# Kernel tuning notes

Hardware: AMD Instinct MI355X
Metric: run time of the kernel (lower is better)

## Reference

```python
import jax, jax.numpy as jnp
import numpy as np

IN_FEAT = 3 * 32 * 32  # channels*height*width
HID = 1024
CLASSES = 10
EPS = 1e-5


def binarize(w):
    # Deterministic BinaryConnect: sign(w) in {-1, +1} (sign(0) -> +1)
    return jnp.where(w >= 0, 1.0, -1.0).astype(w.dtype)


def batchnorm(h, gamma, beta):
    # training-mode BatchNorm1d: biased batch stats over batch axis
    mean = jnp.mean(h, axis=0)
    var = jnp.var(h, axis=0)
    return gamma * (h - mean) * jax.lax.rsqrt(var + EPS) + beta


def setup_inputs() -> dict:
    key = jax.random.key(0)
    ks = jax.random.split(key, 6)
    x = jax.random.normal(ks[0], (8192, 3, 32, 32), dtype=jnp.float32)
    # latent real-valued weights, torch Linear layout [out, in], kaiming-ish scale
    W1 = jax.random.normal(ks[1], (HID, IN_FEAT), dtype=jnp.float32) * (1.0 / np.sqrt(IN_FEAT))
    W2 = jax.random.normal(ks[2], (HID, HID), dtype=jnp.float32) * (1.0 / np.sqrt(HID))
    W3 = jax.random.normal(ks[3], (HID, HID), dtype=jnp.float32) * (1.0 / np.sqrt(HID))
    W4 = jax.random.normal(ks[4], (CLASSES, HID), dtype=jnp.float32) * (1.0 / np.sqrt(HID))
    g1 = jnp.ones((HID,), jnp.float32); b1 = jnp.zeros((HID,), jnp.float32)
    g2 = jnp.ones((HID,), jnp.float32); b2 = jnp.zeros((HID,), jnp.float32)
    g3 = jnp.ones((HID,), jnp.float32); b3 = jnp.zeros((HID,), jnp.float32)
    return {"x": x, "W1": W1, "W2": W2, "W3": W3, "W4": W4,
            "g1": g1, "b1": b1, "g2": g2, "b2": b2, "g3": g3, "b3": b3}


def reference(x, W1, W2, W3, W4, g1, b1, g2, b2, g3, b3):
    h = x.reshape(-1, IN_FEAT)                       # [B, 3072]
    h = jax.nn.relu(h @ binarize(W1).T)              # [B, 1024]
    h = batchnorm(h, g1, b1)
    h = jax.nn.relu(h @ binarize(W2).T)
    h = batchnorm(h, g2, b2)
    h = jax.nn.relu(h @ binarize(W3).T)
    h = batchnorm(h, g3, b3)
    return h @ binarize(W4).T                        # [B, classes]
```

## Files before the change

### kernel.cpp

```cpp
#include <hip/hip_runtime.h>
#include <stdint.h>

typedef unsigned short u16;
typedef __attribute__((ext_vector_type(8))) unsigned short ushort8;
typedef __attribute__((ext_vector_type(4))) unsigned short ushort4v;
typedef __attribute__((ext_vector_type(8))) __bf16 bf16x8;
typedef __attribute__((ext_vector_type(4))) float f32x4;
typedef __attribute__((ext_vector_type(16))) float f32x16;

__device__ __forceinline__ u16 f2bf(float f) {
    union { float f; unsigned int u; } v; v.f = f;
    unsigned int r = v.u + 0x7FFFu + ((v.u >> 16) & 1u);
    return (u16)(r >> 16);
}
__device__ __forceinline__ float bf2f(u16 b) {
    union { unsigned int u; float f; } v; v.u = ((unsigned int)b) << 16;
    return v.f;
}

typedef __attribute__((address_space(1))) const uint32_t* gptr_t;
typedef __attribute__((address_space(3))) uint32_t* lptr_t;
__device__ __forceinline__ void async_copy16(const void* g, void* l) {
    __builtin_amdgcn_global_load_lds((gptr_t)g, (lptr_t)l, 16, 0, 0);
}


__global__ __launch_bounds__(256) void pre_kernel(
    const float* __restrict__ x, const float* __restrict__ W1,
    const float* __restrict__ W4,
    u16* __restrict__ Xb, u16* __restrict__ W1b, u16* __restrict__ W4T)
{
    const int b = blockIdx.x;
    if (b < 12288) {
        int i = b * 256 + threadIdx.x;
        const float4* p = (const float4*)(x + (size_t)i * 8);
        float4 x0 = p[0], x1 = p[1];
        ushort8 o;
        o[0] = f2bf(x0.x); o[1] = f2bf(x0.y); o[2] = f2bf(x0.z); o[3] = f2bf(x0.w);
        o[4] = f2bf(x1.x); o[5] = f2bf(x1.y); o[6] = f2bf(x1.z); o[7] = f2bf(x1.w);
        *(ushort8*)(Xb + (size_t)i * 8) = o;
    } else if (b < 13824) {
        int i = (b - 12288) * 256 + threadIdx.x;
        const float4* p = (const float4*)(W1 + (size_t)i * 8);
        float4 x0 = p[0], x1 = p[1];
        ushort8 o;
        o[0] = x0.x >= 0.f ? 0x3F80 : 0xBF80;
        o[1] = x0.y >= 0.f ? 0x3F80 : 0xBF80;
        o[2] = x0.z >= 0.f ? 0x3F80 : 0xBF80;
        o[3] = x0.w >= 0.f ? 0x3F80 : 0xBF80;
        o[4] = x1.x >= 0.f ? 0x3F80 : 0xBF80;
        o[5] = x1.y >= 0.f ? 0x3F80 : 0xBF80;
        o[6] = x1.z >= 0.f ? 0x3F80 : 0xBF80;
        o[7] = x1.w >= 0.f ? 0x3F80 : 0xBF80;
        *(ushort8*)(W1b + (size_t)i * 8) = o;
    } else {
        int idx = (b - 13824) * 256 + threadIdx.x;
        int k = idx >> 4, c = idx & 15;
        u16 v = 0;
        if (c < 10) v = (W4[(size_t)c * 1024 + k] >= 0.f) ? 0x3F80 : 0xBF80;
        W4T[idx] = v;
    }
}

__global__ __launch_bounds__(256) void rescale_w(
    const float* __restrict__ W, const float* __restrict__ ss,
    u16* __restrict__ Wp, float* __restrict__ bias)
{
    const int lane = threadIdx.x & 63;
    const int wid  = threadIdx.x >> 6;
    const int r    = blockIdx.x * 4 + wid;
    float bsum = 0.f;
    #pragma unroll
    for (int k0 = 0; k0 < 1024; k0 += 256) {
        int k = k0 + lane * 4;
        float4 w  = *(const float4*)(W + (size_t)r * 1024 + k);
        float4 sc = *(const float4*)(ss + k);
        float4 sh = *(const float4*)(ss + 1024 + k);
        ushort4v o;
        o[0] = f2bf(w.x >= 0.f ? sc.x : -sc.x);
        o[1] = f2bf(w.y >= 0.f ? sc.y : -sc.y);
        o[2] = f2bf(w.z >= 0.f ? sc.z : -sc.z);
        o[3] = f2bf(w.w >= 0.f ? sc.w : -sc.w);
        bsum += (w.x >= 0.f ? sh.x : -sh.x) + (w.y >= 0.f ? sh.y : -sh.y)
              + (w.z >= 0.f ? sh.z : -sh.z) + (w.w >= 0.f ? sh.w : -sh.w);
        *(ushort4v*)(Wp + (size_t)r * 1024 + k) = o;
    }
    #pragma unroll
    for (int off = 32; off; off >>= 1) bsum += __shfl_xor(bsum, off, 64);
    if (lane == 0) bias[r] = bsum;
}

__device__ __forceinline__ void xcd_map(int& mm, int& jj) {
    const int d = blockIdx.x + blockIdx.y * gridDim.x;
    mm = (d & 7) + (d >> 6) * 8;
    jj = (d >> 3) & 7;
}


__global__ __launch_bounds__(256) void gemm_fused(
    const u16* __restrict__ A, const u16* __restrict__ B,
    u16* __restrict__ H, const float* __restrict__ bias,
    float* __restrict__ partS, float* __restrict__ partS2,
    int M, int N, int K)
{
    __shared__ __align__(16) u16 As[2][128 * 64];
    __shared__ __align__(16) u16 Bs[2][128 * 64];

    const int tid  = threadIdx.x;
    const int wid  = tid >> 6;
    const int lane = tid & 63;
    const int cl   = lane & 31;
    const int hi   = lane >> 5;
    const int x7r  = cl & 7;
    const int wr   = wid >> 1;
    const int wc   = wid & 1;

    int mm, jj;
    xcd_map(mm, jj);
    const int row0 = mm * 128;
    const int col0 = jj * 128;

    const int s_r = tid >> 3;
    const int s_c = (((tid & 7) ^ (s_r & 7)) << 3);
    const u16* gA = A + (size_t)(row0 + s_r) * K + s_c;
    const u16* gB = B + (size_t)(col0 + s_r) * K + s_c;

    const int a_base0 = (wr * 64 +  0 + cl) * 64;
    const int a_base1 = (wr * 64 + 32 + cl) * 64;
    const int b_base0 = (wc * 64 +  0 + cl) * 64;
    const int b_base1 = (wc * 64 + 32 + cl) * 64;

    f32x16 acc[2][2];
    #pragma unroll
    for (int i = 0; i < 2; ++i)
        #pragma unroll
        for (int j = 0; j < 2; ++j)
            #pragma unroll
            for (int r = 0; r < 16; ++r)
                acc[i][j][r] = 0.f;

    const int NT = K >> 6;

    auto STAGE = [&](int buf, int t) {
        const u16* pa = gA + (size_t)t * 64;
        const u16* pb = gB + (size_t)t * 64;
        #pragma unroll
        for (int i = 0; i < 4; ++i)
            async_copy16(pa + (size_t)i * 32 * K, &As[buf][i * 2048 + wid * 512]);
        #pragma unroll
        for (int i = 0; i < 4; ++i)
            async_copy16(pb + (size_t)i * 32 * K, &Bs[buf][i * 2048 + wid * 512]);
    };

    STAGE(0, 0);
    STAGE(1, 1);

    for (int t = 0; t < NT; ++t) {
        const int buf = t & 1;
        if (t + 1 < NT) asm volatile("s_waitcnt vmcnt(8)" ::: "memory");
        else            asm volatile("s_waitcnt vmcnt(0)" ::: "memory");
        __builtin_amdgcn_s_barrier();

        bf16x8 af0[4], af1[4], bg0[4], bg1[4];
        #pragma unroll
        for (int kt = 0; kt < 4; ++kt) {
            const int xk = ((((kt << 1) | hi) ^ x7r) << 3);
            af0[kt] = *(const bf16x8*)&As[buf][a_base0 + xk];
            af1[kt] = *(const bf16x8*)&As[buf][a_base1 + xk];
            bg0[kt] = *(const bf16x8*)&Bs[buf][b_base0 + xk];
            bg1[kt] = *(const bf16x8*)&Bs[buf][b_base1 + xk];
            __builtin_amdgcn_sched_barrier(0);
        }

        asm volatile("s_waitcnt lgkmcnt(12)" ::: "memory");
        __builtin_amdgcn_sched_barrier(0);
        __builtin_amdgcn_s_setprio(1);
        acc[0][0] = __builtin_amdgcn_mfma_f32_32x32x16_bf16(af0[0], bg0[0], acc[0][0], 0, 0, 0);
        acc[0][1] = __builtin_amdgcn_mfma_f32_32x32x16_bf16(af0[0], bg1[0], acc[0][1], 0, 0, 0);
        acc[1][0] = __builtin_amdgcn_mfma_f32_32x32x16_bf16(af1[0], bg0[0], acc[1][0], 0, 0, 0);
        acc[1][1] = __builtin_amdgcn_mfma_f32_32x32x16_bf16(af1[0], bg1[0], acc[1][1], 0, 0, 0);
        asm volatile("s_waitcnt lgkmcnt(8)" ::: "memory");
        __builtin_amdgcn_sched_barrier(0);
        acc[0][0] = __builtin_amdgcn_mfma_f32_32x32x16_bf16(af0[1], bg0[1], acc[0][0], 0, 0, 0);
        acc[0][1] = __builtin_amdgcn_mfma_f32_32x32x16_bf16(af0[1], bg1[1], acc[0][1], 0, 0, 0);
        acc[1][0] = __builtin_amdgcn_mfma_f32_32x32x16_bf16(af1[1], bg0[1], acc[1][0], 0, 0, 0);
        acc[1][1] = __builtin_amdgcn_mfma_f32_32x32x16_bf16(af1[1], bg1[1], acc[1][1], 0, 0, 0);
        __builtin_amdgcn_s_setprio(0);

        asm volatile("s_waitcnt lgkmcnt(0)" ::: "memory");
        __builtin_amdgcn_sched_barrier(0);
        __builtin_amdgcn_s_barrier();

        if (t + 2 < NT) STAGE(buf, t + 2);

        __builtin_amdgcn_s_setprio(1);
        acc[0][0] = __builtin_amdgcn_mfma_f32_32x32x16_bf16(af0[2], bg0[2], acc[0][0], 0, 0, 0);
        acc[0][1] = __builtin_amdgcn_mfma_f32_32x32x16_bf16(af0[2], bg1[2], acc[0][1], 0, 0, 0);
        acc[1][0] = __builtin_amdgcn_mfma_f32_32x32x16_bf16(af1[2], bg0[2], acc[1][0], 0, 0, 0);
        acc[1][1] = __builtin_amdgcn_mfma_f32_32x32x16_bf16(af1[2], bg1[2], acc[1][1], 0, 0, 0);
        acc[0][0] = __builtin_amdgcn_mfma_f32_32x32x16_bf16(af0[3], bg0[3], acc[0][0], 0, 0, 0);
        acc[0][1] = __builtin_amdgcn_mfma_f32_32x32x16_bf16(af0[3], bg1[3], acc[0][1], 0, 0, 0);
        acc[1][0] = __builtin_amdgcn_mfma_f32_32x32x16_bf16(af1[3], bg0[3], acc[1][0], 0, 0, 0);
        acc[1][1] = __builtin_amdgcn_mfma_f32_32x32x16_bf16(af1[3], bg1[3], acc[1][1], 0, 0, 0);
        __builtin_amdgcn_s_setprio(0);
    }

    #pragma unroll
    for (int j = 0; j < 2; ++j) {
        const int c = col0 + wc * 64 + j * 32 + cl;
        const float bj = bias ? bias[c] : 0.f;
        float s = 0.f, s2 = 0.f;
        #pragma unroll
        for (int i = 0; i < 2; ++i) {
            #pragma unroll
            for (int reg = 0; reg < 16; ++reg) {
                const int rl = (reg & 3) + 8 * (reg >> 2) + 4 * hi;
                const int r = row0 + wr * 64 + i * 32 + rl;
                float x = acc[i][j][reg] + bj;
                x = x > 0.f ? x : 0.f;
                s += x; s2 += x * x;
                H[(size_t)r * N + c] = f2bf(x);
            }
        }
        s  += __shfl_xor(s, 32, 64);
        s2 += __shfl_xor(s2, 32, 64);
        if (hi == 0) {
            const int p = mm * 2 + wr;
            partS [(size_t)p * 1024 + c] = s;
            partS2[(size_t)p * 1024 + c] = s2;
        }
    }
}


__global__ __launch_bounds__(256) void bn_finalize(
    const float* __restrict__ partS, const float* __restrict__ partS2,
    const float* __restrict__ gamma, const float* __restrict__ beta,
    float* __restrict__ ss)
{
    int c = blockIdx.x * 256 + threadIdx.x;
    float s = 0.f, s2 = 0.f;
    for (int i = 0; i < 128; ++i) {
        s  += partS [(size_t)i * 1024 + c];
        s2 += partS2[(size_t)i * 1024 + c];
    }
    float mean = s * (1.0f / 8192.0f);
    float var  = fmaxf(s2 * (1.0f / 8192.0f) - mean * mean, 0.f);
    float sc   = gamma[c] * rsqrtf(var + 1e-5f);
    ss[c]        = sc;
    ss[1024 + c] = beta[c] - mean * sc;
}


__global__ __launch_bounds__(256) void head_kernel(
    const u16* __restrict__ H, const u16* __restrict__ W4T,
    const float* __restrict__ ss, float* __restrict__ out)
{
    const int lane = threadIdx.x & 63;
    const int wid  = threadIdx.x >> 6;
    const int r    = blockIdx.x * 4 + wid;

    float acc[10];
    #pragma unroll
    for (int c = 0; c < 10; c++) acc[c] = 0.f;

    #pragma unroll
    for (int j = 0; j < 16; ++j) {
        int k = j * 64 + lane;
        float a = fmaf(bf2f(H[(size_t)r * 1024 + k]), ss[k], ss[1024 + k]);
        ushort8 w0 = *(const ushort8*)(W4T + (size_t)k * 16);
        acc[0] += a * bf2f(w0[0]); acc[1] += a * bf2f(w0[1]);
        acc[2] += a * bf2f(w0[2]); acc[3] += a * bf2f(w0[3]);
        acc[4] += a * bf2f(w0[4]); acc[5] += a * bf2f(w0[5]);
        acc[6] += a * bf2f(w0[6]); acc[7] += a * bf2f(w0[7]);
        u16 w8 = W4T[(size_t)k * 16 + 8];
        u16 w9 = W4T[(size_t)k * 16 + 9];
        acc[8] += a * bf2f(w8);    acc[9] += a * bf2f(w9);
    }
    #pragma unroll
    for (int c = 0; c < 10; c++) {
        float s = acc[c];
        #pragma unroll
        for (int off = 32; off > 0; off >>= 1) s += __shfl_xor(s, off, 64);
        acc[c] = s;
    }
    if (lane == 0) {
        #pragma unroll
        for (int c = 0; c < 10; c++) out[(size_t)r * 10 + c] = acc[c];
    }
}


extern "C" void kernel_launch(void* const* d_in, const int* in_sizes, int n_in,
                              void* d_out, int out_size, void* d_ws, size_t ws_size,
                              hipStream_t stream) {
    const float* x  = (const float*)d_in[0];
    const float* W1 = (const float*)d_in[1];
    const float* W2 = (const float*)d_in[2];
    const float* W3 = (const float*)d_in[3];
    const float* W4 = (const float*)d_in[4];
    const float* g1 = (const float*)d_in[5];
    const float* b1 = (const float*)d_in[6];
    const float* g2 = (const float*)d_in[7];
    const float* b2 = (const float*)d_in[8];
    const float* g3 = (const float*)d_in[9];
    const float* b3 = (const float*)d_in[10];
    float* out = (float*)d_out;

    char* ws = (char*)d_ws;
    u16*   Xb     = (u16*)  (ws + 0);
    u16*   Hb0    = (u16*)  (ws + 50331648);
    u16*   Hb1    = (u16*)  (ws + 67108864);
    u16*   W1b    = (u16*)  (ws + 83886080);
    u16*   W2p    = (u16*)  (ws + 90177536);
    u16*   W3p    = (u16*)  (ws + 92274688);
    u16*   W4T    = (u16*)  (ws + 94371840);
    float* partS  = (float*)(ws + 94404608);
    float* partS2 = (float*)(ws + 94928896);
    float* ss     = (float*)(ws + 95453184);
    float* bias2  = (float*)(ws + 95461376);
    float* bias3  = (float*)(ws + 95465472);

    pre_kernel<<<13888, 256, 0, stream>>>(x, W1, W4, Xb, W1b, W4T);

    dim3 gemm_grid(64, 8);

    gemm_fused<<<gemm_grid, 256, 0, stream>>>(Xb, W1b, Hb0, nullptr, partS, partS2, 8192, 1024, 3072);
    bn_finalize<<<4, 256, 0, stream>>>(partS, partS2, g1, b1, ss);
    rescale_w<<<256, 256, 0, stream>>>(W2, ss, W2p, bias2);

    gemm_fused<<<gemm_grid, 256, 0, stream>>>(Hb0, W2p, Hb1, bias2, partS, partS2, 8192, 1024, 1024);
    bn_finalize<<<4, 256, 0, stream>>>(partS, partS2, g2, b2, ss);
    rescale_w<<<256, 256, 0, stream>>>(W3, ss, W3p, bias3);

    gemm_fused<<<gemm_grid, 256, 0, stream>>>(Hb1, W3p, Hb0, bias3, partS, partS2, 8192, 1024, 1024);
    bn_finalize<<<4, 256, 0, stream>>>(partS, partS2, g3, b3, ss);

    head_kernel<<<2048, 256, 0, stream>>>(Hb0, W4T, ss, out);
}
```

Before: 197.2 us.

## Double-buffer register fragments and change LDS swizzle to cut bank conflicts

Restructures the GEMM main loop so that the LDS fragment reads for the next k-tile are issued in the middle of the current tile's MFMA sequence. Two register fragment sets (P/Q) alternate across a loop unrolled by two. It also changes the XOR swizzle to include row>>3 plus a per-row-group flip, aiming to reduce LDS bank conflicts on the 16-byte reads. This hides LDS read latency behind matrix math at the cost of roughly doubling fragment register usage. The loop assumes NT is even.

```diff
diff --git a/kernel.cpp b/kernel.cpp
--- a/kernel.cpp
+++ b/kernel.cpp
@@ -5,7 +5,6 @@
 typedef __attribute__((ext_vector_type(8))) unsigned short ushort8;
 typedef __attribute__((ext_vector_type(4))) unsigned short ushort4v;
 typedef __attribute__((ext_vector_type(8))) __bf16 bf16x8;
-typedef __attribute__((ext_vector_type(4))) float f32x4;
 typedef __attribute__((ext_vector_type(16))) float f32x16;
 
 __device__ __forceinline__ u16 f2bf(float f) {
@@ -111,7 +110,6 @@
     const int lane = tid & 63;
     const int cl   = lane & 31;
     const int hi   = lane >> 5;
-    const int x7r  = cl & 7;
     const int wr   = wid >> 1;
     const int wc   = wid & 1;
 
@@ -121,89 +119,110 @@
     const int col0 = jj * 128;
 
     const int s_r = tid >> 3;
-    const int s_c = (((tid & 7) ^ (s_r & 7)) << 3);
-    const u16* gA = A + (size_t)(row0 + s_r) * K + s_c;
-    const u16* gB = B + (size_t)(col0 + s_r) * K + s_c;
+    const int c8b = (tid & 7) ^ (s_r & 7) ^ (s_r >> 3);
+    const u16* gA = A + (size_t)(row0 + s_r) * K;
+    const u16* gB = B + (size_t)(col0 + s_r) * K;
 
     const int a_base0 = (wr * 64 +  0 + cl) * 64;
     const int a_base1 = (wr * 64 + 32 + cl) * 64;
     const int b_base0 = (wc * 64 +  0 + cl) * 64;
     const int b_base1 = (wc * 64 + 32 + cl) * 64;
-
-    f32x16 acc[2][2];
-    #pragma unroll
-    for (int i = 0; i < 2; ++i)
-        #pragma unroll
-        for (int j = 0; j < 2; ++j)
-            #pragma unroll
-            for (int r = 0; r < 16; ++r)
-                acc[i][j][r] = 0.f;
+    const int rho0 = (cl & 7) ^ (cl >> 3);
+    int xk0[4], xk1[4];
+    #pragma unroll
+    for (int kt = 0; kt < 4; ++kt) {
+        xk0[kt] = ((((kt << 1) | hi) ^ rho0) << 3);
+        xk1[kt] = xk0[kt] ^ 32;
+    }
+
+    f32x16 acc00, acc01, acc10, acc11;
+    #pragma unroll
+    for (int r = 0; r < 16; ++r) { acc00[r]=0.f; acc01[r]=0.f; acc10[r]=0.f; acc11[r]=0.f; }
 
     const int NT = K >> 6;
 
     auto STAGE = [&](int buf, int t) {
-        const u16* pa = gA + (size_t)t * 64;
-        const u16* pb = gB + (size_t)t * 64;
-        #pragma unroll
-        for (int i = 0; i < 4; ++i)
-            async_copy16(pa + (size_t)i * 32 * K, &As[buf][i * 2048 + wid * 512]);
-        #pragma unroll
-        for (int i = 0; i < 4; ++i)
-            async_copy16(pb + (size_t)i * 32 * K, &Bs[buf][i * 2048 + wid * 512]);
+        #pragma unroll
+        for (int i = 0; i < 4; ++i) {
+            const int co = (c8b ^ ((i & 1) << 2)) << 3;
+            async_copy16(gA + ((size_t)i * 32) * K + (size_t)t * 64 + co,
+                         &As[buf][i * 2048 + wid * 512]);
+        }
+        #pragma unroll
+        for (int i = 0; i < 4; ++i) {
+            const int co = (c8b ^ ((i & 1) << 2)) << 3;
+            async_copy16(gB + ((size_t)i * 32) * K + (size_t)t * 64 + co,
+                         &Bs[buf][i * 2048 + wid * 512]);
+        }
     };
+
+    bf16x8 pa0[4], pa1[4], pb0[4], pb1[4];
+    bf16x8 qa0[4], qa1[4], qb0[4], qb1[4];
+
+#define READ_P(buf)                                                   \
+    _Pragma("unroll")                                                 \
+    for (int kt = 0; kt < 4; ++kt) {                                  \
+        pa0[kt] = *(const bf16x8*)&As[buf][a_base0 + xk0[kt]];        \
+        pa1[kt] = *(const bf16x8*)&As[buf][a_base1 + xk1[kt]];        \
+        pb0[kt] = *(const bf16x8*)&Bs[buf][b_base0 + xk0[kt]];        \
+        pb1[kt] = *(const bf16x8*)&Bs[buf][b_base1 + xk1[kt]];        \
+    }
+#define READ_Q(buf)                                                   \
+    _Pragma("unroll")                                                 \
+    for (int kt = 0; kt < 4; ++kt) {                                  \
+        qa0[kt] = *(const bf16x8*)&As[buf][a_base0 + xk0[kt]];        \
+        qa1[kt] = *(const bf16x8*)&As[buf][a_base1 + xk1[kt]];        \
+        qb0[kt] = *(const bf16x8*)&Bs[buf][b_base0 + xk0[kt]];        \
+        qb1[kt] = *(const bf16x8*)&Bs[buf][b_base1 + xk1[kt]];        \
+    }
+#define MFMA4(SA0, SA1, SB0, SB1, kt)                                                      \
+    acc00 = __builtin_amdgcn_mfma_f32_32x32x16_bf16(SA0[kt], SB0[kt], acc00, 0, 0, 0);     \
+    acc01 = __builtin_amdgcn_mfma_f32_32x32x16_bf16(SA0[kt], SB1[kt], acc01, 0, 0, 0);     \
+    acc10 = __builtin_amdgcn_mfma_f32_32x32x16_bf16(SA1[kt], SB0[kt], acc10, 0, 0, 0);     \
+    acc11 = __builtin_amdgcn_mfma_f32_32x32x16_bf16(SA1[kt], SB1[kt], acc11, 0, 0, 0);
 
     STAGE(0, 0);
     STAGE(1, 1);
-
-    for (int t = 0; t < NT; ++t) {
-        const int buf = t & 1;
-        if (t + 1 < NT) asm volatile("s_waitcnt vmcnt(8)" ::: "memory");
-        else            asm volatile("s_waitcnt vmcnt(0)" ::: "memory");
-        __builtin_amdgcn_s_barrier();
-
-        bf16x8 af0[4], af1[4], bg0[4], bg1[4];
-        #pragma unroll
-        for (int kt = 0; kt < 4; ++kt) {
-            const int xk = ((((kt << 1) | hi) ^ x7r) << 3);
-            af0[kt] = *(const bf16x8*)&As[buf][a_base0 + xk];
-            af1[kt] = *(const bf16x8*)&As[buf][a_base1 + xk];
-            bg0[kt] = *(const bf16x8*)&Bs[buf][b_base0 + xk];
-            bg1[kt] = *(const bf16x8*)&Bs[buf][b_base1 + xk];
-            __builtin_amdgcn_sched_barrier(0);
-        }
-
-        asm volatile("s_waitcnt lgkmcnt(12)" ::: "memory");
-        __builtin_amdgcn_sched_barrier(0);
-        __builtin_amdgcn_s_setprio(1);
-        acc[0][0] = __builtin_amdgcn_mfma_f32_32x32x16_bf16(af0[0], bg0[0], acc[0][0], 0, 0, 0);
-        acc[0][1] = __builtin_amdgcn_mfma_f32_32x32x16_bf16(af0[0], bg1[0], acc[0][1], 0, 0, 0);
-        acc[1][0] = __builtin_amdgcn_mfma_f32_32x32x16_bf16(af1[0], bg0[0], acc[1][0], 0, 0, 0);
-        acc[1][1] = __builtin_amdgcn_mfma_f32_32x32x16_bf16(af1[0], bg1[0], acc[1][1], 0, 0, 0);
-        asm volatile("s_waitcnt lgkmcnt(8)" ::: "memory");
-        __builtin_amdgcn_sched_barrier(0);
-        acc[0][0] = __builtin_amdgcn_mfma_f32_32x32x16_bf16(af0[1], bg0[1], acc[0][0], 0, 0, 0);
-        acc[0][1] = __builtin_amdgcn_mfma_f32_32x32x16_bf16(af0[1], bg1[1], acc[0][1], 0, 0, 0);
-        acc[1][0] = __builtin_amdgcn_mfma_f32_32x32x16_bf16(af1[1], bg0[1], acc[1][0], 0, 0, 0);
-        acc[1][1] = __builtin_amdgcn_mfma_f32_32x32x16_bf16(af1[1], bg1[1], acc[1][1], 0, 0, 0);
-        __builtin_amdgcn_s_setprio(0);
-
-        asm volatile("s_waitcnt lgkmcnt(0)" ::: "memory");
-        __builtin_amdgcn_sched_barrier(0);
-        __builtin_amdgcn_s_barrier();
-
-        if (t + 2 < NT) STAGE(buf, t + 2);
-
-        __builtin_amdgcn_s_setprio(1);
-        acc[0][0] = __builtin_amdgcn_mfma_f32_32x32x16_bf16(af0[2], bg0[2], acc[0][0], 0, 0, 0);
-        acc[0][1] = __builtin_amdgcn_mfma_f32_32x32x16_bf16(af0[2], bg1[2], acc[0][1], 0, 0, 0);
-        acc[1][0] = __builtin_amdgcn_mfma_f32_32x32x16_bf16(af1[2], bg0[2], acc[1][0], 0, 0, 0);
-        acc[1][1] = __builtin_amdgcn_mfma_f32_32x32x16_bf16(af1[2], bg1[2], acc[1][1], 0, 0, 0);
-        acc[0][0] = __builtin_amdgcn_mfma_f32_32x32x16_bf16(af0[3], bg0[3], acc[0][0], 0, 0, 0);
-        acc[0][1] = __builtin_amdgcn_mfma_f32_32x32x16_bf16(af0[3], bg1[3], acc[0][1], 0, 0, 0);
-        acc[1][0] = __builtin_amdgcn_mfma_f32_32x32x16_bf16(af1[3], bg0[3], acc[1][0], 0, 0, 0);
-        acc[1][1] = __builtin_amdgcn_mfma_f32_32x32x16_bf16(af1[3], bg1[3], acc[1][1], 0, 0, 0);
-        __builtin_amdgcn_s_setprio(0);
-    }
+    asm volatile("s_waitcnt vmcnt(8)" ::: "memory");
+    __builtin_amdgcn_s_barrier();
+    READ_P(0)
+    asm volatile("s_waitcnt lgkmcnt(0)" ::: "memory");
+    __builtin_amdgcn_sched_barrier(0);
+    __builtin_amdgcn_s_barrier();
+
+#define G_ITER(T, MA0, MA1, MB0, MB1, READ_N)                                 \
+    {                                                                         \
+        const int bufc = (T) & 1;                                             \
+        if ((T) + 2 < NT) STAGE(bufc, (T) + 2);                               \
+        __builtin_amdgcn_s_setprio(1);                                        \
+        MFMA4(MA0, MA1, MB0, MB1, 0)                                          \
+        MFMA4(MA0, MA1, MB0, MB1, 1)                                          \
+        __builtin_amdgcn_s_setprio(0);                                        \
+        if ((T) + 1 < NT) {                                                   \
+            if ((T) + 2 < NT) asm volatile("s_waitcnt vmcnt(8)" ::: "memory");\
+            else              asm volatile("s_waitcnt vmcnt(0)" ::: "memory");\
+            __builtin_amdgcn_s_barrier();                                     \
+            READ_N(((T) + 1) & 1)                                             \
+        }                                                                     \
+        __builtin_amdgcn_s_setprio(1);                                        \
+        MFMA4(MA0, MA1, MB0, MB1, 2)                                          \
+        MFMA4(MA0, MA1, MB0, MB1, 3)                                          \
+        __builtin_amdgcn_s_setprio(0);                                        \
+        if ((T) + 1 < NT) {                                                   \
+            asm volatile("s_waitcnt lgkmcnt(0)" ::: "memory");                \
+            __builtin_amdgcn_sched_barrier(0);                                \
+            __builtin_amdgcn_s_barrier();                                     \
+        }                                                                     \
+    }
+
+    for (int t2 = 0; t2 < NT; t2 += 2) {
+        G_ITER(t2,     pa0, pa1, pb0, pb1, READ_Q)
+        G_ITER(t2 + 1, qa0, qa1, qb0, qb1, READ_P)
+    }
+#undef G_ITER
+#undef MFMA4
+#undef READ_P
+#undef READ_Q
 
     #pragma unroll
     for (int j = 0; j < 2; ++j) {
@@ -216,7 +235,8 @@
             for (int reg = 0; reg < 16; ++reg) {
                 const int rl = (reg & 3) + 8 * (reg >> 2) + 4 * hi;
                 const int r = row0 + wr * 64 + i * 32 + rl;
-                float x = acc[i][j][reg] + bj;
+                float x = (i == 0 ? (j == 0 ? acc00[reg] : acc01[reg])
+                                  : (j == 0 ? acc10[reg] : acc11[reg])) + bj;
                 x = x > 0.f ? x : 0.f;
                 s += x; s2 += x * x;
                 H[(size_t)r * N + c] = f2bf(x);
```

After: 260.7 us. 1.32x slower.
